# Kernel optimization log

Hardware: AMD Instinct MI355X
Metric: run time of the kernel (lower is better)

The kernel has to match this reference:

```python
import jax, jax.numpy as jnp
import numpy as np

B, T, IN = 32, 64, 90
U, SEG = 4, 16          # conductor steps, decoder steps per segment (T = U*SEG)
H1, HC, HD, Z = 2048, 1024, 1024, 512


def _lstm_layer(x, wih, whh, bih, bhh, h0=None, c0=None, reverse=False):
    """PyTorch-convention LSTM layer. x: [B,T,D]. Returns (ys [B,T,H], final h [B,H])."""
    b = x.shape[0]
    H = whh.shape[1]
    # precompute input projection for all timesteps: [T,B,4H]
    xp = jnp.swapaxes(jnp.einsum('btd,gd->btg', x, wih) + bih, 0, 1)
    if h0 is None:
        h0 = jnp.zeros((b, H), x.dtype)
        c0 = h0
    def step(carry, xt):
        h, c = carry
        g = xt + h @ whh.T + bhh
        i, f, gg, o = jnp.split(g, 4, axis=-1)  # torch gate order i,f,g,o
        c = jax.nn.sigmoid(f) * c + jax.nn.sigmoid(i) * jnp.tanh(gg)
        h = jax.nn.sigmoid(o) * jnp.tanh(c)
        return (h, c), h
    (h, c), ys = jax.lax.scan(step, (h0, c0), xp, reverse=reverse)
    return jnp.swapaxes(ys, 0, 1), h


def _cell(xin, h, c, wih, whh, bih, bhh):
    g = xin @ wih.T + bih + h @ whh.T + bhh
    i, f, gg, o = jnp.split(g, 4, axis=-1)
    c = jax.nn.sigmoid(f) * c + jax.nn.sigmoid(i) * jnp.tanh(gg)
    h = jax.nn.sigmoid(o) * jnp.tanh(c)
    return h, c


def setup_inputs() -> dict:
    key = jax.random.key(0)
    ks = iter(jax.random.split(key, 64))
    def p(*shape):
        return jax.random.normal(next(ks), shape, dtype=jnp.float32) * 0.02
    inp = {}
    inp['x'] = jax.random.normal(next(ks), (B, T, IN), dtype=jnp.float32)
    inp['eps'] = jax.random.normal(next(ks), (B, Z), dtype=jnp.float32)
    # encoder bi-LSTM: 2 layers x 2 directions
    for name, d in [('e0f', IN), ('e0b', IN), ('e1f', 2 * H1), ('e1b', 2 * H1)]:
        inp[name + '_wih'] = p(4 * H1, d)
        inp[name + '_whh'] = p(4 * H1, H1)
        inp[name + '_bih'] = p(4 * H1)
        inp[name + '_bhh'] = p(4 * H1)
    inp['wm'] = p(Z, 2 * H1); inp['bm'] = p(Z)
    inp['ws'] = p(Z, 2 * H1); inp['bs'] = p(Z)
    inp['w2'] = p(4 * HC, Z); inp['b2'] = p(4 * HC)
    # conductor LSTM: 2 layers, input size 1
    for name, d in [('c0', 1), ('c1', HC)]:
        inp[name + '_wih'] = p(4 * HC, d)
        inp[name + '_whh'] = p(4 * HC, HC)
        inp[name + '_bih'] = p(4 * HC)
        inp[name + '_bhh'] = p(4 * HC)
    inp['w3'] = p(4 * HD, HC); inp['b3'] = p(4 * HD)
    # two decoder LSTMCells
    for name, d in [('d1', HC + IN), ('d2', HD)]:
        inp[name + '_wih'] = p(4 * HD, d)
        inp[name + '_whh'] = p(4 * HD, HD)
        inp[name + '_bih'] = p(4 * HD)
        inp[name + '_bhh'] = p(4 * HD)
    inp['w4'] = p(IN, HD); inp['b4'] = p(IN)
    return inp


def reference(x, eps,
              e0f_wih, e0f_whh, e0f_bih, e0f_bhh,
              e0b_wih, e0b_whh, e0b_bih, e0b_bhh,
              e1f_wih, e1f_whh, e1f_bih, e1f_bhh,
              e1b_wih, e1b_whh, e1b_bih, e1b_bhh,
              wm, bm, ws, bs, w2, b2,
              c0_wih, c0_whh, c0_bih, c0_bhh,
              c1_wih, c1_whh, c1_bih, c1_bhh,
              w3, b3,
              d1_wih, d1_whh, d1_bih, d1_bhh,
              d2_wih, d2_whh, d2_bih, d2_bhh,
              w4, b4):
    b = x.shape[0]
    # ----- encode: 2-layer bidirectional LSTM, take layer-1 fwd/bwd final h -----
    y0f, _ = _lstm_layer(x, e0f_wih, e0f_whh, e0f_bih, e0f_bhh)
    y0b, _ = _lstm_layer(x, e0b_wih, e0b_whh, e0b_bih, e0b_bhh, reverse=True)
    y0 = jnp.concatenate([y0f, y0b], axis=2)  # [B,T,2*H1]
    _, hf = _lstm_layer(y0, e1f_wih, e1f_whh, e1f_bih, e1f_bhh)
    _, hb = _lstm_layer(y0, e1b_wih, e1b_whh, e1b_bih, e1b_bhh, reverse=True)
    ht = jnp.concatenate([hf, hb], axis=1)  # [B,4096]
    z_mean = ht @ wm.T + bm
    z_std = jnp.log1p(jnp.exp(ht @ ws.T + bs))  # softplus as in source
    z = z_mean + eps * z_std
    # ----- conductor -----
    t = jnp.tanh(z @ w2.T + b2)
    h1, h2, c1, c2 = jnp.split(t, 4, axis=1)  # source order: h1,h2,c1,c2
    zin = jnp.zeros((b, U, 1), x.dtype)
    yc0, _ = _lstm_layer(zin, c0_wih, c0_whh, c0_bih, c0_bhh, h1, c1)
    emb, _ = _lstm_layer(yc0, c1_wih, c1_whh, c1_bih, c1_bhh, h2, c2)  # [B,U,HC]
    def segment(prev, e):
        s = jnp.tanh(e @ w3.T + b3)
        sh1, sh2, sc1, sc2 = jnp.split(s, 4, axis=1)
        def step(carry, _):
            dh1, dc1, dh2, dc2, p = carry
            inp = jnp.concatenate([e, p], axis=1)
            dh1, dc1 = _cell(inp, dh1, dc1, d1_wih, d1_whh, d1_bih, d1_bhh)
            dh2, dc2 = _cell(dh1, dh2, dc2, d2_wih, d2_whh, d2_bih, d2_bhh)
            p = dh2 @ w4.T + b4
            return (dh1, dc1, dh2, dc2, p), p
        carry, outs = jax.lax.scan(step, (sh1, sc1, sh2, sc2, prev), None, length=SEG)
        return carry[4], outs  # outs: [SEG,B,IN]
    prev0 = jnp.zeros((b, IN), x.dtype)
    _, outs = jax.lax.scan(segment, prev0, jnp.swapaxes(emb, 0, 1))  # [U,SEG,B,IN]
    out = jnp.transpose(outs.reshape(U * SEG, b, IN), (1, 0, 2))  # [B,T,IN]
    out = jax.nn.softmax(out, axis=2)
    return out, z_mean, z_std
```

## Files before the change

kernel.cpp:

```cpp
#include <hip/hip_runtime.h>
#include <hip/hip_cooperative_groups.h>
#include <math.h>

#define BB 32
#define TT 64
#define INPW 90
#define NU 4
#define NH1 2048
#define NHC 1024
#define NHD 1024
#define NZ 512
#define BSTRIDE 12800

typedef unsigned short u16;
typedef __attribute__((ext_vector_type(8))) short short8;
typedef __attribute__((ext_vector_type(4))) float f32x4;
typedef __attribute__((ext_vector_type(4))) unsigned uv4;
typedef __attribute__((ext_vector_type(2))) unsigned uv2;

__device__ __forceinline__ float sigf(float v) { return 1.0f / (1.0f + __expf(-v)); }

__device__ __forceinline__ u16 f2bf(float f) {
  unsigned u = __float_as_uint(f);
  unsigned r = (u + 0x7FFFu + ((u >> 16) & 1u)) >> 16;
  return (u16)r;
}
__device__ __forceinline__ float bf2f(u16 b) { return __uint_as_float(((unsigned)b) << 16); }

__device__ __forceinline__ void cstore16(u16* p, uv4 v) {
  asm volatile("global_store_dwordx4 %0, %1, off sc0 sc1" :: "v"(p), "v"(v) : "memory");
}
__device__ __forceinline__ void cstore8(u16* p, uv2 v) {
  asm volatile("global_store_dwordx2 %0, %1, off sc0 sc1" :: "v"(p), "v"(v) : "memory");
}
__device__ __forceinline__ void cstore4(unsigned* p, unsigned v) {
  asm volatile("global_store_dword %0, %1, off sc0 sc1" :: "v"(p), "v"(v) : "memory");
}
__device__ __forceinline__ unsigned fload(const unsigned* p) {
  unsigned r;
  asm volatile("global_load_dword %0, %1, off sc0 sc1\n\ts_waitcnt vmcnt(0)"
               : "=v"(r) : "v"(p) : "memory");
  return r;
}
__device__ __forceinline__ void gbar(unsigned* base) {
  asm volatile("s_waitcnt vmcnt(0)" ::: "memory");
  __syncthreads();
  if (threadIdx.x == 0) {
    unsigned old = atomicAdd(&base[(blockIdx.x & 15) * 512], 1u);
    if (old == 15u) {
      unsigned m = atomicAdd(&base[16 * 512], 1u);
      if (m == 15u) {
#pragma unroll
        for (int k = 0; k < 8; ++k) cstore4(&base[(17 + k) * 512], 1u);
        asm volatile("s_waitcnt vmcnt(0)" ::: "memory");
      }
    }
    while (!fload(&base[(17 + (blockIdx.x & 7)) * 512])) __builtin_amdgcn_s_sleep(2);
  }
  __syncthreads();
}

__device__ __forceinline__ void gload16(const u16* g, u16* l) {
  __builtin_amdgcn_global_load_lds(
      (const __attribute__((address_space(1))) unsigned*)g,
      (__attribute__((address_space(3))) unsigned*)l, 16, 0, 0);
}

__global__ void cvt_flat(const float* __restrict__ s, u16* __restrict__ d, long n) {
  long i = ((long)blockIdx.x * 256 + threadIdx.x) * 4;
  if (i >= n) return;
  float4 v = *(const float4*)&s[i];
  d[i] = f2bf(v.x); d[i + 1] = f2bf(v.y); d[i + 2] = f2bf(v.z); d[i + 3] = f2bf(v.w);
}

__global__ void cvt_pad(const float* __restrict__ s, int sld, int cols,
                        u16* __restrict__ d, int dld, int rows) {
  int c = blockIdx.x * blockDim.x + threadIdx.x;
  int r = blockIdx.y;
  if (c >= dld) return;
  d[(long)r * dld + c] = (c < cols) ? f2bf(s[(long)r * sld + c]) : (u16)0;
}

__global__ void cvt_permrow(const float* __restrict__ s, int sld, int cols,
                            u16* __restrict__ d, int dld, int H) {
  int c = blockIdx.x * blockDim.x + threadIdx.x;
  int r = blockIdx.y;
  if (c >= dld) return;
  long sr = (long)(r & 3) * H + (r >> 2);
  d[(long)r * dld + c] = (c < cols) ? f2bf(s[sr * sld + c]) : (u16)0;
}

__global__ void bias_perm(const float* __restrict__ s, float* __restrict__ d, int H) {
  int n = blockIdx.x * 256 + threadIdx.x;
  if (n >= 4 * H) return;
  d[n] = s[(long)(n & 3) * H + (n >> 2)];
}

__global__ void xcvt(const float* __restrict__ x, u16* __restrict__ xb) {
  int r = blockIdx.x, c = threadIdx.x;
  int b = r & 31, t = r >> 5;
  float v = (c < INPW) ? x[((long)b * TT + t) * INPW + c] : 0.0f;
  xb[(long)r * 128 + c] = f2bf(v);
}

__global__ void w4t_k(const float* __restrict__ w4, u16* __restrict__ w4tb) {
  int k = blockIdx.x, n = threadIdx.x;
  w4tb[(long)k * 128 + n] = (n < INPW) ? f2bf(w4[(long)n * NHD + k]) : (u16)0;
}

__global__ void bfuse_k(const float* __restrict__ d1_wih, const float* __restrict__ b4,
                        float* __restrict__ bfuse) {
  int r = blockIdx.x * 256 + threadIdx.x;
  if (r >= 4096) return;
  float s = 0.0f;
  for (int n = 0; n < INPW; ++n) s += d1_wih[(long)r * 1114 + 1024 + n] * b4[n];
  bfuse[r] = s;
}

__global__ __launch_bounds__(256) void gemm_bf(
    const u16* __restrict__ A, int lda, const u16* __restrict__ Bw, int ldb,
    const float* __restrict__ bias, u16* __restrict__ C, int ldc, int K, int mode,
    int nbm, int nbn) {
  __shared__ u16 Asm[2][128 * 64];
  __shared__ u16 Bsm[2][128 * 64];
  const int tid = threadIdx.x;
  const int w = tid >> 6, l = tid & 63, q = (tid >> 4) & 3, ln = tid & 15;
  const int wm = w & 1, wn = w >> 1;
  int fid = blockIdx.x;
  int sidx = fid >> 3, xcd = fid & 7;
  int bm, bn;
  if ((nbm & 7) == 0) { bn = sidx % nbn; bm = xcd * (nbm >> 3) + sidx / nbn; }
  else if ((nbn & 7) == 0) { bm = sidx % nbm; bn = xcd * (nbn >> 3) + sidx / nbm; }
  else { bm = fid % nbm; bn = fid / nbm; }
  const long am0 = (long)bm * 128;
  const long bn0 = (long)bn * 128;
  const u16* Ap0 = A + am0 * lda;
  const u16* Bp0 = Bw + bn0 * ldb;
  f32x4 acc[4][4] = {};

  auto stage = [&](int b, int k0) {
#pragma unroll
    for (int i = 0; i < 4; ++i) {
      int row = (w * 4 + i) * 8 + (l >> 3);
      int col = (((l & 7) ^ (row & 7)) << 3) + k0;
      gload16(Ap0 + (long)row * lda + col, &Asm[b][(w * 4 + i) * 512]);
      gload16(Bp0 + (long)row * ldb + col, &Bsm[b][(w * 4 + i) * 512]);
    }
  };

  const int kt = K >> 6;
  stage(0, 0);
  asm volatile("s_waitcnt vmcnt(0)" ::: "memory");
  __syncthreads();
  int buf = 0;
  for (int t = 0; t < kt; ++t) {
    if (t + 1 < kt) stage(buf ^ 1, (t + 1) << 6);
#pragma unroll
    for (int kh = 0; kh < 2; ++kh) {
      short8 af[4], bg[4];
#pragma unroll
      for (int tt2 = 0; tt2 < 4; ++tt2) {
        int arr = wm * 64 + tt2 * 16 + ln;
        af[tt2] = *(short8*)&Asm[buf][arr * 64 + (((q + 4 * kh) ^ (arr & 7)) << 3)];
        int brr = wn * 64 + tt2 * 16 + ln;
        bg[tt2] = *(short8*)&Bsm[buf][brr * 64 + (((q + 4 * kh) ^ (brr & 7)) << 3)];
      }
#pragma unroll
      for (int mt = 0; mt < 4; ++mt)
#pragma unroll
        for (int nt = 0; nt < 4; ++nt)
          acc[mt][nt] = __builtin_amdgcn_mfma_f32_16x16x32_bf16(af[mt], bg[nt], acc[mt][nt], 0, 0, 0);
    }
    asm volatile("s_waitcnt vmcnt(0)" ::: "memory");
    __syncthreads();
    buf ^= 1;
  }
#pragma unroll
  for (int nt = 0; nt < 4; ++nt) {
    long n = bn0 + wn * 64 + nt * 16 + ln;
    float bv = bias ? bias[n] : 0.0f;
#pragma unroll
    for (int mt = 0; mt < 4; ++mt) {
#pragma unroll
      for (int r = 0; r < 4; ++r) {
        long m = am0 + wm * 64 + mt * 16 + (q << 2) + r;
        long dst;
        if (mode == 0) {
          dst = m * ldc + n;
        } else if (mode == 1) {
          dst = (((m >> 5) * 256 + (n >> 5)) * 32 + (m & 31)) * 32 + (n & 31);
        } else {
          dst = ((n >> 4) * 128 + m) * 16 + (n & 15);
        }
        C[dst] = f2bf(acc[mt][nt][r] + bv);
      }
    }
  }
}

__global__ __launch_bounds__(256) void gemm128(
    const float* __restrict__ A, int lda, const float* __restrict__ W, int ldw,
    const float* __restrict__ bias, float* __restrict__ C, int ldc,
    int M, int K, int act, u16* __restrict__ Cb) {
  __shared__ float As[16][132];
  __shared__ float Bs[16][132];
  const int tid = threadIdx.x;
  const int bm = blockIdx.x, bn = blockIdx.y;
  const int tm = tid & 15, tn = tid >> 4;
  float acc[8][8] = {};
  for (int k0 = 0; k0 < K; k0 += 16) {
#pragma unroll
    for (int it = 0; it < 2; ++it) {
      int e = it * 256 + tid;
      int r = e >> 2, c4 = (e & 3) * 4;
      int m = bm * 128 + r;
      float4 v = make_float4(0.f, 0.f, 0.f, 0.f);
      if (m < M) v = *(const float4*)&A[(long)m * lda + k0 + c4];
      As[c4 + 0][r] = v.x; As[c4 + 1][r] = v.y; As[c4 + 2][r] = v.z; As[c4 + 3][r] = v.w;
      int n = bn * 128 + r;
      float4 w = *(const float4*)&W[(long)n * ldw + k0 + c4];
      Bs[c4 + 0][r] = w.x; Bs[c4 + 1][r] = w.y; Bs[c4 + 2][r] = w.z; Bs[c4 + 3][r] = w.w;
    }
    __syncthreads();
#pragma unroll
    for (int kk = 0; kk < 16; ++kk) {
      float4 a0 = *(const float4*)&As[kk][tm * 8];
      float4 a1 = *(const float4*)&As[kk][tm * 8 + 4];
      float4 b0 = *(const float4*)&Bs[kk][tn * 8];
      float4 b1 = *(const float4*)&Bs[kk][tn * 8 + 4];
      float av[8] = {a0.x, a0.y, a0.z, a0.w, a1.x, a1.y, a1.z, a1.w};
      float bv[8] = {b0.x, b0.y, b0.z, b0.w, b1.x, b1.y, b1.z, b1.w};
#pragma unroll
      for (int i = 0; i < 8; ++i)
#pragma unroll
        for (int j = 0; j < 8; ++j)
          acc[i][j] += av[i] * bv[j];
    }
    __syncthreads();
  }
#pragma unroll
  for (int i = 0; i < 8; ++i) {
    int m = bm * 128 + tm * 8 + i;
    if (m >= M) continue;
#pragma unroll
    for (int j = 0; j < 8; ++j) {
      int n = bn * 128 + tn * 8 + j;
      float v = acc[i][j] + bias[n];
      if (act == 1) v = tanhf(v);
      else if (act == 2) v = log1pf(__expf(v));
      C[(long)m * ldc + n] = v;
      if (Cb) Cb[(long)m * ldc + n] = f2bf(v);
    }
  }
}

__global__ __launch_bounds__(256) void latgemm(
    const float* __restrict__ A, const float* __restrict__ W,
    const float* __restrict__ bias, float* __restrict__ C, int act) {
  __shared__ float red[16][16][32];
  const int tid = threadIdx.x;
  const int c = tid & 15, ksl = tid >> 4;
  const int n = blockIdx.x * 16 + c;
  const float* wp = W + (long)n * 4096 + ksl * 256;
  const float* ap = A + ksl * 256;
  float acc[32];
#pragma unroll
  for (int r = 0; r < 32; ++r) acc[r] = 0.f;
  for (int k = 0; k < 256; k += 4) {
    float4 wv = *(const float4*)(wp + k);
#pragma unroll
    for (int r = 0; r < 32; ++r) {
      float4 hv = *(const float4*)(ap + (long)r * 4096 + k);
      acc[r] += hv.x * wv.x + hv.y * wv.y + hv.z * wv.z + hv.w * wv.w;
    }
  }
#pragma unroll
  for (int r = 0; r < 32; ++r) red[ksl][c][r] = acc[r];
  __syncthreads();
  for (int o = tid; o < 512; o += 256) {
    int cc = o >> 5, r = o & 31;
    float s = 0.f;
#pragma unroll
    for (int p = 0; p < 16; ++p) s += red[p][cc][r];
    s += bias[blockIdx.x * 16 + cc];
    if (act == 2) s = log1pf(__expf(s));
    C[(long)r * 512 + blockIdx.x * 16 + cc] = s;
  }
}

__global__ void zcalc_kernel(const float* __restrict__ zm, const float* __restrict__ zs,
                             const float* __restrict__ eps, float* __restrict__ z) {
  int e = blockIdx.x * 256 + threadIdx.x;
  if (e < BB * NZ) z[e] = zm[e] + eps[e] * zs[e];
}

__global__ void softmax_kernel(float* __restrict__ out) {
  long row = blockIdx.x;
  float* p = out + row * INPW;
  int lane = threadIdx.x;
  float v0 = (lane < INPW) ? p[lane] : -1e30f;
  float v1 = (lane + 64 < INPW) ? p[lane + 64] : -1e30f;
  float m = fmaxf(v0, v1);
#pragma unroll
  for (int off = 32; off > 0; off >>= 1) m = fmaxf(m, __shfl_xor(m, off));
  float e0 = (lane < INPW) ? __expf(v0 - m) : 0.0f;
  float e1 = (lane + 64 < INPW) ? __expf(v1 - m) : 0.0f;
  float sum = e0 + e1;
#pragma unroll
  for (int off = 32; off > 0; off >>= 1) sum += __shfl_xor(sum, off);
  float inv = 1.0f / sum;
  if (lane < INPW) p[lane] = e0 * inv;
  if (lane + 64 < INPW) p[lane + 64] = e1 * inv;
}

struct EncArgs {
  const u16* whh[2];
  const u16* xp[2];
  const float* bhh[2];
  u16* y0b;
  u16* h1a[2];
  float* htb;
  unsigned* bar;
  int layer;
};

__global__ __launch_bounds__(512) void enc_coop(EncArgs A) {
  __shared__ u16 Wl[2 * 64 * 64 * 8];
  __shared__ __align__(16) float red[4 * 64 * 4];
  __shared__ __align__(16) u16 hstage[32][8];
  const int tid = threadIdx.x;
  const int w = tid >> 6, l = tid & 63;
  const int rt = w & 1, bh = (w >> 1) & 1, kh = w >> 2;
  const int kg = l >> 4, b0 = l & 15;
  const int j0 = blockIdx.x * 8;
  const int jout = j0 + rt * 4 + kg;
  const int batch = bh * 16 + b0;
  float* redp = &red[((bh * 2 + rt) * 64 + l) * 4];

  for (int dir = 0; dir < 2; ++dir) {
    __syncthreads();
    {
      const u16* W = A.whh[dir];
      for (int e = tid; e < 8192; e += 512) {
        int ert = e >> 12, es = (e >> 6) & 63, el = e & 63;
        int etr = el & 15;
        long gr = (long)(etr & 3) * 2048 + j0 + ert * 4 + (etr >> 2);
        *(uint4*)&Wl[((ert * 64 + es) * 64 + el) * 8] =
            *(const uint4*)&W[gr * 2048 + (el >> 4) * 8 + (long)es * 32];
      }
    }
    __syncthreads();
    const float* bhh = A.bhh[dir];
    const u16* xp = A.xp[dir];
    const float bi0 = bhh[jout], bi1 = bhh[2048 + jout],
                bi2 = bhh[4096 + jout], bi3 = bhh[6144 + jout];
    float creg = 0.f;
    ushort4 xv4 = make_ushort4(0, 0, 0, 0);
    if (kh == 0) {
      int tt0 = dir ? 63 : 0;
      xv4 = *(const ushort4*)(xp + ((((long)tt0 * 256 + blockIdx.x) * 32 + batch) * 32)
                              + (rt * 4 + kg) * 4);
    }
    for (int s = 0; s < 64; ++s) {
      if (s) gbar(A.bar + (long)(dir * 63 + (s - 1)) * BSTRIDE);
      const int tt = dir ? 63 - s : s;
      f32x4 acc = {0.f, 0.f, 0.f, 0.f};
      if (s) {
        const u16* hb; long hld;
        if (A.layer == 0) {
          int tp = dir ? tt + 1 : tt - 1;
          hb = A.y0b + (long)tp * 32 * 4096 + dir * 2048;
          hld = 4096;
        } else {
          hb = A.h1a[dir] + (long)(s - 1) * 32 * 2048;
          hld = 2048;
        }
        const u16* xv = hb + (long)batch * hld + kg * 8;
        for (int ks = kh * 32; ks < kh * 32 + 32; ks += 8) {
          uint4 bv[8]; short8 av[8];
#pragma unroll
          for (int uu = 0; uu < 8; ++uu)
            bv[uu] = *(const uint4*)(xv + (long)(ks + uu) * 32);
#pragma unroll
          for (int uu = 0; uu < 8; ++uu)
            av[uu] = *(const short8*)&Wl[((rt * 64 + ks + uu) * 64 + l) * 8];
#pragma unroll
          for (int uu = 0; uu < 8; ++uu)
            acc = __builtin_amdgcn_mfma_f32_16x16x32_bf16(av[uu], *(short8*)&bv[uu], acc, 0, 0, 0);
        }
      }
      if (kh) *(f32x4*)redp = acc;
      __syncthreads();
      if (kh == 0) {
        f32x4 o = *(f32x4*)redp;
        float g0 = acc[0] + o[0] + bi0 + bf2f(xv4.x);
        float g1 = acc[1] + o[1] + bi1 + bf2f(xv4.y);
        float g2 = acc[2] + o[2] + bi2 + bf2f(xv4.z);
        float g3 = acc[3] + o[3] + bi3 + bf2f(xv4.w);
        float iv = sigf(g0), fv = sigf(g1), gv = tanhf(g2), ov = sigf(g3);
        float c = fv * creg + iv * gv;
        creg = c;
        float h = ov * tanhf(c);
        hstage[batch][rt * 4 + kg] = f2bf(h);
        if (A.layer == 1 && s == 63) A.htb[batch * 4096 + dir * 2048 + jout] = h;
      }
      __syncthreads();
      if (tid < 32) {
        uv4 v = *(const uv4*)&hstage[tid][0];
        u16* dst;
        if (A.layer == 0) dst = &A.y0b[((long)tt * 32 + tid) * 4096 + dir * 2048 + j0];
        else dst = &A.h1a[dir][((long)s * 32 + tid) * 2048 + j0];
        cstore16(dst, v);
      }
      if (kh == 0 && s < 63) {
        int ttn = dir ? 62 - s : s + 1;
        xv4 = *(const ushort4*)(xp + ((((long)ttn * 256 + blockIdx.x) * 32 + batch) * 32)
                                + (rt * 4 + kg) * 4);
      }
    }
  }
}

__device__ __forceinline__ void stage_w1024(u16* Wl, int m, const u16* W, int j0, int tid) {
  for (int e = tid; e < 2048; e += 512) {
    int kh = e >> 10, s = (e >> 6) & 15, el = e & 63;
    int tr = el & 15;
    long gr = (long)(tr & 3) * 1024 + j0 + (tr >> 2);
    *(uint4*)&Wl[(((m * 2 + kh) * 16 + s) * 64 + el) * 8] =
        *(const uint4*)&W[gr * 1024 + kh * 512 + (el >> 4) * 8 + s * 32];
  }
}

__device__ __forceinline__ void cell1024_lds(
    const u16* Wl, int m0, int m1,
    int j0, int tid, float* red, u16* hstage,
    const u16* X0, long x0ld,
    const u16* X1, long x1ld,
    float xg0, float xg1, float xg2, float xg3,
    float b0, float b1, float b2, float b3,
    float co, float* crp,
    u16* hout, long hld, float* houtf, long hfld) {
  const int w = tid >> 6, l = tid & 63;
  const int bh = w & 1, kh = w >> 1;
  const int kg = l >> 4;
  const int koff = kh * 256 + kg * 8;
  const int batch = bh * 16 + (l & 15);
  const int sbase = (kh >> 1) * 16 + (kh & 1) * 8;
  const int jout = j0 + kg;
  f32x4 acc = {0.f, 0.f, 0.f, 0.f};
  if (X0) {
    const u16* xpt = X0 + (long)batch * x0ld + koff;
    const int sb = m0 * 32 + sbase;
    uint4 bv[8]; short8 av[8];
#pragma unroll
    for (int uu = 0; uu < 8; ++uu) bv[uu] = *(const uint4*)(xpt + (long)uu * 32);
#pragma unroll
    for (int uu = 0; uu < 8; ++uu) av[uu] = *(const short8*)&Wl[((sb + uu) * 64 + l) * 8];
#pragma unroll
    for (int uu = 0; uu < 8; ++uu)
      acc = __builtin_amdgcn_mfma_f32_16x16x32_bf16(av[uu], *(short8*)&bv[uu], acc, 0, 0, 0);
  }
  if (X1) {
    const u16* xpt = X1 + (long)batch * x1ld + koff;
    const int sb = m1 * 32 + sbase;
    uint4 bv[8]; short8 av[8];
#pragma unroll
    for (int uu = 0; uu < 8; ++uu) bv[uu] = *(const uint4*)(xpt + (long)uu * 32);
#pragma unroll
    for (int uu = 0; uu < 8; ++uu) av[uu] = *(const short8*)&Wl[((sb + uu) * 64 + l) * 8];
#pragma unroll
    for (int uu = 0; uu < 8; ++uu)
      acc = __builtin_amdgcn_mfma_f32_16x16x32_bf16(av[uu], *(short8*)&bv[uu], acc, 0, 0, 0);
  }
  if (kh) *(f32x4*)&red[((kh - 1) * 2 + bh) * 256 + l * 4] = acc;
  __syncthreads();
  if (kh == 0) {
#pragma unroll
    for (int p = 0; p < 3; ++p) {
      f32x4 o = *(f32x4*)&red[(p * 2 + bh) * 256 + l * 4];
      acc[0] += o[0]; acc[1] += o[1]; acc[2] += o[2]; acc[3] += o[3];
    }
    float g0 = acc[0] + b0 + xg0;
    float g1 = acc[1] + b1 + xg1;
    float g2 = acc[2] + b2 + xg2;
    float g3 = acc[3] + b3 + xg3;
    float iv = sigf(g0), fv = sigf(g1), gv = tanhf(g2), ov = sigf(g3);
    float c = fv * co + iv * gv;
    *crp = c;
    float h = ov * tanhf(c);
    hstage[batch * 4 + kg] = f2bf(h);
    if (houtf) houtf[(long)batch * hfld + jout] = h;
  }
  __syncthreads();
  if (tid < 32) {
    uv2 v = *(const uv2*)&hstage[tid * 4];
    cstore8(&hout[(long)tid * hld + j0], v);
  }
}

struct CondArgs {
  const u16 *c0h, *c1w, *c1h, *tvecb;
  const float* tvec;
  u16 *yc0b, *embb;
  float* embf;
  const float *b0i, *b0h, *b1i, *b1h;
  unsigned* bar;
};
__global__ __launch_bounds__(512) void cond_coop(CondArgs A) {
  __shared__ u16 Wl[3 * 32 * 512];
  __shared__ __align__(16) float red[6 * 256];
  __shared__ __align__(16) u16 hstage[128];
  const int j0 = blockIdx.x * 4;
  const int tid = threadIdx.x;
  const int w = tid >> 6, l = tid & 63;
  const int bh = w & 1;
  const int jout = j0 + (l >> 4);
  const int batch = bh * 16 + (l & 15);
  stage_w1024(Wl, 0, A.c0h, j0, tid);
  stage_w1024(Wl, 1, A.c1w, j0, tid);
  stage_w1024(Wl, 2, A.c1h, j0, tid);
  const float cb00 = A.b0i[jout] + A.b0h[jout];
  const float cb01 = A.b0i[1024 + jout] + A.b0h[1024 + jout];
  const float cb02 = A.b0i[2048 + jout] + A.b0h[2048 + jout];
  const float cb03 = A.b0i[3072 + jout] + A.b0h[3072 + jout];
  const float cb10 = A.b1i[jout] + A.b1h[jout];
  const float cb11 = A.b1i[1024 + jout] + A.b1h[1024 + jout];
  const float cb12 = A.b1i[2048 + jout] + A.b1h[2048 + jout];
  const float cb13 = A.b1i[3072 + jout] + A.b1h[3072 + jout];
  const float c0init = A.tvec[2048 + (long)batch * 4096 + jout];
  const float c1init = A.tvec[3072 + (long)batch * 4096 + jout];
  __syncthreads();
  float cr0 = c0init, cr1 = c1init;
  int bi = 0;
  for (int u = 0; u < NU; ++u) {
    cell1024_lds(Wl, 0, -1, j0, tid, red, hstage,
                 u ? A.yc0b + (long)(u - 1) * 32 * 1024 : A.tvecb, u ? 1024 : 4096,
                 nullptr, 0,
                 0.f, 0.f, 0.f, 0.f,
                 cb00, cb01, cb02, cb03,
                 cr0, &cr0,
                 A.yc0b + (long)u * 32 * 1024, 1024, nullptr, 0);
    gbar(A.bar + (long)(bi++) * BSTRIDE);
    cell1024_lds(Wl, 1, 2, j0, tid, red, hstage,
                 A.yc0b + (long)u * 32 * 1024, 1024,
                 u ? A.embb + (long)(u - 1) * 32 * 1024 : A.tvecb + 1024, u ? 1024 : 4096,
                 0.f, 0.f, 0.f, 0.f,
                 cb10, cb11, cb12, cb13,
                 cr1, &cr1,
                 A.embb + (long)u * 32 * 1024, 1024, A.embf + (long)u * 32 * 1024, 1024);
    if (u < NU - 1) gbar(A.bar + (long)(bi++) * BSTRIDE);
  }
}

struct DecArgs {
  const u16 *d1h, *wfuse, *d2w, *d2h, *xeb, *sallb;
  const float* sall;
  u16 *dh1all, *dh2all;
  const float *bfuse, *b1h, *b2i, *b2h;
  unsigned* bar;
};
__global__ __launch_bounds__(512) void dec_coop(DecArgs A) {
  __shared__ u16 Wl[4 * 32 * 512];
  __shared__ __align__(16) float red[6 * 256];
  __shared__ __align__(16) u16 hstage[128];
  const int j0 = blockIdx.x * 4;
  const int tid = threadIdx.x;
  const int w = tid >> 6, l = tid & 63;
  const int bh = w & 1;
  const int kg = l >> 4;
  const int jout = j0 + kg;
  const int batch = bh * 16 + (l & 15);
  stage_w1024(Wl, 0, A.d1h, j0, tid);
  stage_w1024(Wl, 1, A.wfuse, j0, tid);
  stage_w1024(Wl, 2, A.d2w, j0, tid);
  stage_w1024(Wl, 3, A.d2h, j0, tid);
  const float b1z0 = A.b1h[jout], b1z1 = A.b1h[1024 + jout],
              b1z2 = A.b1h[2048 + jout], b1z3 = A.b1h[3072 + jout];
  const float b1n0 = b1z0 + A.bfuse[jout], b1n1 = b1z1 + A.bfuse[1024 + jout],
              b1n2 = b1z2 + A.bfuse[2048 + jout], b1n3 = b1z3 + A.bfuse[3072 + jout];
  const float b20 = A.b2i[jout] + A.b2h[jout];
  const float b21 = A.b2i[1024 + jout] + A.b2h[1024 + jout];
  const float b22 = A.b2i[2048 + jout] + A.b2h[2048 + jout];
  const float b23 = A.b2i[3072 + jout] + A.b2h[3072 + jout];
  const u16* xqb = A.xeb + (long)blockIdx.x * 128 * 16;
  ushort4 xq4 = *(const ushort4*)(xqb + (long)batch * 16 + kg * 4);
  float con1 = A.sall[(long)batch * 4096 + 2048 + jout];
  float con2 = A.sall[(long)batch * 4096 + 3072 + jout];
  __syncthreads();
  float cr1 = 0.f, cr2 = 0.f;
  int bi = 0;
  for (int t = 0; t < TT; ++t) {
    const int u = t >> 4, sg = t & 15;
    if (sg == 0) { cr1 = con1; cr2 = con2; }
    cell1024_lds(Wl, 0, 1, j0, tid, red, hstage,
                 sg ? A.dh1all + (long)(t - 1) * 32 * 1024 : A.sallb + (long)u * 32 * 4096,
                 sg ? 1024 : 4096,
                 t ? A.dh2all + (long)(t - 1) * 32 * 1024 : nullptr, 1024,
                 bf2f(xq4.x), bf2f(xq4.y), bf2f(xq4.z), bf2f(xq4.w),
                 t ? b1n0 : b1z0, t ? b1n1 : b1z1, t ? b1n2 : b1z2, t ? b1n3 : b1z3,
                 cr1, &cr1,
                 A.dh1all + (long)t * 32 * 1024, 1024, nullptr, 0);
    gbar(A.bar + (long)(bi++) * BSTRIDE);
    cell1024_lds(Wl, 2, 3, j0, tid, red, hstage,
                 A.dh1all + (long)t * 32 * 1024, 1024,
                 sg ? A.dh2all + (long)(t - 1) * 32 * 1024 : A.sallb + (long)u * 32 * 4096 + 1024,
                 sg ? 1024 : 4096,
                 0.f, 0.f, 0.f, 0.f,
                 b20, b21, b22, b23,
                 cr2, &cr2,
                 A.dh2all + (long)t * 32 * 1024, 1024, nullptr, 0);
    if (sg == 15 && u < 3) {
      xq4 = *(const ushort4*)(xqb + (long)(u + 1) * 32 * 16 + (long)batch * 16 + kg * 4);
      con1 = A.sall[(long)(u + 1) * 32 * 4096 + (long)batch * 4096 + 2048 + jout];
      con2 = A.sall[(long)(u + 1) * 32 * 4096 + (long)batch * 4096 + 3072 + jout];
    }
    if (t < TT - 1) gbar(A.bar + (long)(bi++) * BSTRIDE);
  }
}

__global__ __launch_bounds__(256) void proj_all(const u16* __restrict__ dh2all,
                                                const u16* __restrict__ w4b,
                                                const float* __restrict__ b4,
                                                float* __restrict__ out) {
  __shared__ u16 hs[8 * 1024];
  const int r0 = blockIdx.x * 8;
  for (int e = threadIdx.x; e < 1024; e += 256)
    ((uint4*)hs)[e] = ((const uint4*)(dh2all + (long)r0 * 1024))[e];
  __syncthreads();
  for (int o = threadIdx.x; o < 8 * INPW; o += 256) {
    int rr = o / INPW, n = o % INPW;
    const u16* wr = w4b + (long)n * 1024;
    const u16* hr = hs + rr * 1024;
    float s = 0.0f;
    for (int k = 0; k < 1024; ++k) s += bf2f(hr[k]) * bf2f(wr[k]);
    int row = r0 + rr;
    int tt = row >> 5, b = row & 31;
    out[((long)b * TT + tt) * INPW + n] = s + b4[n];
  }
}

extern "C" void kernel_launch(void* const* d_in, const int* in_sizes, int n_in,
                              void* d_out, int out_size, void* d_ws, size_t ws_size,
                              hipStream_t stream) {
  (void)in_sizes; (void)n_in; (void)out_size;
  const float* x        = (const float*)d_in[0];
  const float* eps      = (const float*)d_in[1];
  const float* e0f_wih  = (const float*)d_in[2];
  const float* e0f_whh  = (const float*)d_in[3];
  const float* e0f_bih  = (const float*)d_in[4];
  const float* e0f_bhh  = (const float*)d_in[5];
  const float* e0b_wih  = (const float*)d_in[6];
  const float* e0b_whh  = (const float*)d_in[7];
  const float* e0b_bih  = (const float*)d_in[8];
  const float* e0b_bhh  = (const float*)d_in[9];
  const float* e1f_wih  = (const float*)d_in[10];
  const float* e1f_whh  = (const float*)d_in[11];
  const float* e1f_bih  = (const float*)d_in[12];
  const float* e1f_bhh  = (const float*)d_in[13];
  const float* e1b_wih  = (const float*)d_in[14];
  const float* e1b_whh  = (const float*)d_in[15];
  const float* e1b_bih  = (const float*)d_in[16];
  const float* e1b_bhh  = (const float*)d_in[17];
  const float* wm  = (const float*)d_in[18];
  const float* bm  = (const float*)d_in[19];
  const float* wsw = (const float*)d_in[20];
  const float* bsv = (const float*)d_in[21];
  const float* w2  = (const float*)d_in[22];
  const float* b2  = (const float*)d_in[23];
  const float* c0_whh = (const float*)d_in[25];
  const float* c0_bih = (const float*)d_in[26];
  const float* c0_bhh = (const float*)d_in[27];
  const float* c1_wih = (const float*)d_in[28];
  const float* c1_whh = (const float*)d_in[29];
  const float* c1_bih = (const float*)d_in[30];
  const float* c1_bhh = (const float*)d_in[31];
  const float* w3 = (const float*)d_in[32];
  const float* b3 = (const float*)d_in[33];
  const float* d1_wih = (const float*)d_in[34];
  const float* d1_whh = (const float*)d_in[35];
  const float* d1_bih = (const float*)d_in[36];
  const float* d1_bhh = (const float*)d_in[37];
  const float* d2_wih = (const float*)d_in[38];
  const float* d2_whh = (const float*)d_in[39];
  const float* d2_bih = (const float*)d_in[40];
  const float* d2_bhh = (const float*)d_in[41];
  const float* w4 = (const float*)d_in[42];
  const float* b4 = (const float*)d_in[43];

  float* out = (float*)d_out;
  float* zm_out = out + (size_t)BB * TT * INPW;
  float* zs_out = zm_out + BB * NZ;

  char* wbase = (char*)d_ws;
  size_t cur = 0;
  auto AL = [&](size_t bytes) -> void* {
    void* p = wbase + cur;
    cur = (cur + bytes + 255) & ~(size_t)255;
    return p;
  };
  u16* xb    = (u16*)AL(2048L * 128 * 2);
  u16* e0wf  = (u16*)AL(8192L * 128 * 2);
  u16* e0wb  = (u16*)AL(8192L * 128 * 2);
  u16* e0hf  = (u16*)AL(8192L * 2048 * 2);
  u16* e0hb  = (u16*)AL(8192L * 2048 * 2);
  u16* e1wf  = (u16*)AL(8192L * 4096 * 2);
  u16* e1wb  = (u16*)AL(8192L * 4096 * 2);
  u16* e1hf  = (u16*)AL(8192L * 2048 * 2);
  u16* e1hb  = (u16*)AL(8192L * 2048 * 2);
  u16* c0h   = (u16*)AL(4096L * 1024 * 2);
  u16* c1w   = (u16*)AL(4096L * 1024 * 2);
  u16* c1h   = (u16*)AL(4096L * 1024 * 2);
  u16* d1we  = (u16*)AL(4096L * 1024 * 2);
  u16* d1wp  = (u16*)AL(4096L * 128 * 2);
  u16* d1h   = (u16*)AL(4096L * 1024 * 2);
  u16* d2w   = (u16*)AL(4096L * 1024 * 2);
  u16* d2h   = (u16*)AL(4096L * 1024 * 2);
  u16* w4b   = (u16*)AL(90L * 1024 * 2);
  u16* w4tb  = (u16*)AL(1024L * 128 * 2);
  u16* wfuse = (u16*)AL(4096L * 1024 * 2);
  float* bfuse = (float*)AL(4096L * 4);
  float* pb_e0f = (float*)AL(8192L * 4);
  float* pb_e0b = (float*)AL(8192L * 4);
  float* pb_e1f = (float*)AL(8192L * 4);
  float* pb_e1b = (float*)AL(8192L * 4);
  float* pb_d1  = (float*)AL(4096L * 4);
  u16* xp0f  = (u16*)AL(2048L * 8192 * 2);
  u16* xp0b  = (u16*)AL(2048L * 8192 * 2);
  u16* y0b   = (u16*)AL(2048L * 4096 * 2);
  u16* xp1f  = (u16*)AL(2048L * 8192 * 2);
  u16* xp1b  = (u16*)AL(2048L * 8192 * 2);
  u16* h1af  = (u16*)AL(64L * 32 * 2048 * 2);
  u16* h1ab  = (u16*)AL(64L * 32 * 2048 * 2);
  u16* tvecb = (u16*)AL(32L * 4096 * 2);
  u16* yc0b  = (u16*)AL(4L * 32 * 1024 * 2);
  u16* embb  = (u16*)AL(4L * 32 * 1024 * 2);
  u16* sallb = (u16*)AL(128L * 4096 * 2);
  u16* xeb   = (u16*)AL(128L * 4096 * 2);
  u16* dh1all= (u16*)AL(64L * 32 * 1024 * 2);
  u16* dh2all= (u16*)AL(64L * 32 * 1024 * 2);
  float* htb  = (float*)AL(32L * 4096 * 4);
  float* zbuf = (float*)AL(32L * 512 * 4);
  float* tvec = (float*)AL(32L * 4096 * 4);
  float* embf = (float*)AL(128L * 1024 * 4);
  float* sall = (float*)AL(128L * 4096 * 4);
  unsigned* barp = (unsigned*)AL(400L * BSTRIDE * 4);
  if (cur > ws_size) return;

  unsigned* bar_enc0 = barp;
  unsigned* bar_enc1 = barp + 128L * BSTRIDE;
  unsigned* bar_cond = barp + 256L * BSTRIDE;
  unsigned* bar_dec  = barp + 264L * BSTRIDE;

  auto cf = [&](const float* s, u16* d, long n) {
    cvt_flat<<<dim3((unsigned)((n / 4 + 255) / 256)), 256, 0, stream>>>(s, d, n);
  };
  cf(e0f_whh, e0hf, 8192L * 2048);
  cf(e0b_whh, e0hb, 8192L * 2048);
  cf(e1f_whh, e1hf, 8192L * 2048);
  cf(e1b_whh, e1hb, 8192L * 2048);
  cf(c0_whh, c0h, 4096L * 1024);
  cf(c1_wih, c1w, 4096L * 1024);
  cf(c1_whh, c1h, 4096L * 1024);
  cf(d1_whh, d1h, 4096L * 1024);
  cf(d2_wih, d2w, 4096L * 1024);
  cf(d2_whh, d2h, 4096L * 1024);
  cf(w4, w4b, 90L * 1024);
  cvt_permrow<<<dim3(1, 8192), 128, 0, stream>>>(e0f_wih, 90, 90, e0wf, 128, 2048);
  cvt_permrow<<<dim3(1, 8192), 128, 0, stream>>>(e0b_wih, 90, 90, e0wb, 128, 2048);
  cvt_permrow<<<dim3(16, 8192), 256, 0, stream>>>(e1f_wih, 4096, 4096, e1wf, 4096, 2048);
  cvt_permrow<<<dim3(16, 8192), 256, 0, stream>>>(e1b_wih, 4096, 4096, e1wb, 4096, 2048);
  cvt_permrow<<<dim3(4, 4096), 256, 0, stream>>>(d1_wih, 1114, 1024, d1we, 1024, 1024);
  bias_perm<<<dim3(32), 256, 0, stream>>>(e0f_bih, pb_e0f, 2048);
  bias_perm<<<dim3(32), 256, 0, stream>>>(e0b_bih, pb_e0b, 2048);
  bias_perm<<<dim3(32), 256, 0, stream>>>(e1f_bih, pb_e1f, 2048);
  bias_perm<<<dim3(32), 256, 0, stream>>>(e1b_bih, pb_e1b, 2048);
  bias_perm<<<dim3(16), 256, 0, stream>>>(d1_bih, pb_d1, 1024);
  cvt_pad<<<dim3(1, 4096), 128, 0, stream>>>(d1_wih + 1024, 1114, 90, d1wp, 128, 4096);
  xcvt<<<dim3(2048), 128, 0, stream>>>(x, xb);
  w4t_k<<<dim3(1024), 128, 0, stream>>>(w4, w4tb);
  bfuse_k<<<dim3(16), 256, 0, stream>>>(d1_wih, b4, bfuse);
  hipMemsetAsync(barp, 0, 400L * BSTRIDE * 4, stream);

  gemm_bf<<<dim3(256), 256, 0, stream>>>(d1wp, 128, w4tb, 128, nullptr, wfuse, 1024, 128, 0, 32, 8);
  gemm_bf<<<dim3(1024), 256, 0, stream>>>(xb, 128, e0wf, 128, pb_e0f, xp0f, 8192, 128, 1, 16, 64);
  gemm_bf<<<dim3(1024), 256, 0, stream>>>(xb, 128, e0wb, 128, pb_e0b, xp0b, 8192, 128, 1, 16, 64);

  {
    EncArgs ea{};
    ea.whh[0] = e0hf; ea.whh[1] = e0hb;
    ea.xp[0] = xp0f; ea.xp[1] = xp0b;
    ea.bhh[0] = e0f_bhh; ea.bhh[1] = e0b_bhh;
    ea.y0b = y0b; ea.h1a[0] = h1af; ea.h1a[1] = h1ab; ea.htb = htb;
    ea.bar = bar_enc0; ea.layer = 0;
    void* args[] = {&ea};
    (void)hipLaunchCooperativeKernel((void*)enc_coop, dim3(256), dim3(512), args, 0, stream);
  }

  gemm_bf<<<dim3(1024), 256, 0, stream>>>(y0b, 4096, e1wf, 4096, pb_e1f, xp1f, 8192, 4096, 1, 16, 64);
  gemm_bf<<<dim3(1024), 256, 0, stream>>>(y0b, 4096, e1wb, 4096, pb_e1b, xp1b, 8192, 4096, 1, 16, 64);

  {
    EncArgs ea{};
    ea.whh[0] = e1hf; ea.whh[1] = e1hb;
    ea.xp[0] = xp1f; ea.xp[1] = xp1b;
    ea.bhh[0] = e1f_bhh; ea.bhh[1] = e1b_bhh;
    ea.y0b = y0b; ea.h1a[0] = h1af; ea.h1a[1] = h1ab; ea.htb = htb;
    ea.bar = bar_enc1; ea.layer = 1;
    void* args[] = {&ea};
    (void)hipLaunchCooperativeKernel((void*)enc_coop, dim3(256), dim3(512), args, 0, stream);
  }

  latgemm<<<dim3(32), 256, 0, stream>>>(htb, wm, bm, zm_out, 0);
  latgemm<<<dim3(32), 256, 0, stream>>>(htb, wsw, bsv, zs_out, 2);
  zcalc_kernel<<<dim3(64), 256, 0, stream>>>(zm_out, zs_out, eps, zbuf);
  gemm128<<<dim3(1, 32), 256, 0, stream>>>(zbuf, 512, w2, 512, b2, tvec, 4096, 32, 512, 1, tvecb);

  {
    CondArgs ca{};
    ca.c0h = c0h; ca.c1w = c1w; ca.c1h = c1h;
    ca.tvecb = tvecb; ca.tvec = tvec;
    ca.yc0b = yc0b; ca.embb = embb; ca.embf = embf;
    ca.b0i = c0_bih; ca.b0h = c0_bhh; ca.b1i = c1_bih; ca.b1h = c1_bhh;
    ca.bar = bar_cond;
    void* args[] = {&ca};
    (void)hipLaunchCooperativeKernel((void*)cond_coop, dim3(256), dim3(512), args, 0, stream);
  }

  gemm128<<<dim3(1, 32), 256, 0, stream>>>(embf, 1024, w3, 1024, b3, sall, 4096, 128, 1024, 1, sallb);
  gemm_bf<<<dim3(32), 256, 0, stream>>>(embb, 1024, d1we, 1024, pb_d1, xeb, 4096, 1024, 2, 1, 32);

  {
    DecArgs da{};
    da.d1h = d1h; da.wfuse = wfuse; da.d2w = d2w; da.d2h = d2h;
    da.xeb = xeb; da.sallb = sallb; da.sall = sall;
    da.dh1all = dh1all; da.dh2all = dh2all;
    da.bfuse = bfuse; da.b1h = d1_bhh; da.b2i = d2_bih; da.b2h = d2_bhh;
    da.bar = bar_dec;
    void* args[] = {&da};
    (void)hipLaunchCooperativeKernel((void*)dec_coop, dim3(256), dim3(512), args, 0, stream);
  }

  proj_all<<<dim3(256), 256, 0, stream>>>(dh2all, w4b, b4, out);
  softmax_kernel<<<dim3(BB * TT), 64, 0, stream>>>(out);
}
```

Before: 4.900 ms.

## Replace LDS h staging with wave shuffles and batch conversion launches

The recurrent cells no longer stage each new hidden state in shared memory followed by a block barrier. Instead, lanes gather bf16 h values with wave shuffles, and 16 lanes per wave write 8-byte coherent stores directly, which removes one __syncthreads per cell step on the latency-bound recurrent path. Separately, eleven weight conversion launches are merged into one grid-stride kernel and five bias-permutation launches into one, to reduce launch overhead. The encoder now issues more, smaller stores (dwordx2 instead of dwordx4).

```diff
diff --git a/kernel.cpp b/kernel.cpp
--- a/kernel.cpp
+++ b/kernel.cpp
@@ -27,9 +27,6 @@
 }
 __device__ __forceinline__ float bf2f(u16 b) { return __uint_as_float(((unsigned)b) << 16); }
 
-__device__ __forceinline__ void cstore16(u16* p, uv4 v) {
-  asm volatile("global_store_dwordx4 %0, %1, off sc0 sc1" :: "v"(p), "v"(v) : "memory");
-}
 __device__ __forceinline__ void cstore8(u16* p, uv2 v) {
   asm volatile("global_store_dwordx2 %0, %1, off sc0 sc1" :: "v"(p), "v"(v) : "memory");
 }
@@ -66,11 +63,25 @@
       (__attribute__((address_space(3))) unsigned*)l, 16, 0, 0);
 }
 
-__global__ void cvt_flat(const float* __restrict__ s, u16* __restrict__ d, long n) {
-  long i = ((long)blockIdx.x * 256 + threadIdx.x) * 4;
-  if (i >= n) return;
-  float4 v = *(const float4*)&s[i];
-  d[i] = f2bf(v.x); d[i + 1] = f2bf(v.y); d[i + 2] = f2bf(v.z); d[i + 3] = f2bf(v.w);
+struct CvtJobs { const float* s[12]; u16* d[12]; long n[12]; int cnt; };
+__global__ void cvt_multi(CvtJobs J) {
+  long stride = (long)gridDim.x * 256 * 4;
+  for (int j = 0; j < J.cnt; ++j) {
+    const float* s = J.s[j]; u16* d = J.d[j]; long n = J.n[j];
+    for (long i = ((long)blockIdx.x * 256 + threadIdx.x) * 4; i < n; i += stride) {
+      float4 v = *(const float4*)&s[i];
+      d[i] = f2bf(v.x); d[i + 1] = f2bf(v.y); d[i + 2] = f2bf(v.z); d[i + 3] = f2bf(v.w);
+    }
+  }
+}
+
+struct BPJobs { const float* s[5]; float* d[5]; int H[5]; int cnt; };
+__global__ void bias_perm5(BPJobs J) {
+  for (int j = 0; j < J.cnt; ++j) {
+    int tot = 4 * J.H[j];
+    for (int n = blockIdx.x * 256 + threadIdx.x; n < tot; n += gridDim.x * 256)
+      J.d[j][n] = J.s[j][(long)(n & 3) * J.H[j] + (n >> 2)];
+  }
 }
 
 __global__ void cvt_pad(const float* __restrict__ s, int sld, int cols,
@@ -88,12 +99,6 @@
   if (c >= dld) return;
   long sr = (long)(r & 3) * H + (r >> 2);
   d[(long)r * dld + c] = (c < cols) ? f2bf(s[sr * sld + c]) : (u16)0;
-}
-
-__global__ void bias_perm(const float* __restrict__ s, float* __restrict__ d, int H) {
-  int n = blockIdx.x * 256 + threadIdx.x;
-  if (n >= 4 * H) return;
-  d[n] = s[(long)(n & 3) * H + (n >> 2)];
 }
 
 __global__ void xcvt(const float* __restrict__ x, u16* __restrict__ xb) {
@@ -327,7 +332,6 @@
 __global__ __launch_bounds__(512) void enc_coop(EncArgs A) {
   __shared__ u16 Wl[2 * 64 * 64 * 8];
   __shared__ __align__(16) float red[4 * 64 * 4];
-  __shared__ __align__(16) u16 hstage[32][8];
   const int tid = threadIdx.x;
   const int w = tid >> 6, l = tid & 63;
   const int rt = w & 1, bh = (w >> 1) & 1, kh = w >> 2;
@@ -401,21 +405,27 @@
         float c = fv * creg + iv * gv;
         creg = c;
         float h = ov * tanhf(c);
-        hstage[batch][rt * 4 + kg] = f2bf(h);
         if (A.layer == 1 && s == 63) A.htb[batch * 4096 + dir * 2048 + jout] = h;
-      }
-      __syncthreads();
-      if (tid < 32) {
-        uv4 v = *(const uv4*)&hstage[tid][0];
-        u16* dst;
-        if (A.layer == 0) dst = &A.y0b[((long)tt * 32 + tid) * 4096 + dir * 2048 + j0];
-        else dst = &A.h1a[dir][((long)s * 32 + tid) * 2048 + j0];
-        cstore16(dst, v);
-      }
-      if (kh == 0 && s < 63) {
-        int ttn = dir ? 62 - s : s + 1;
-        xv4 = *(const ushort4*)(xp + ((((long)ttn * 256 + blockIdx.x) * 32 + batch) * 32)
-                                + (rt * 4 + kg) * 4);
+        unsigned hbits = f2bf(h);
+        unsigned p0 = __shfl((int)hbits, (l & 15));
+        unsigned p1 = __shfl((int)hbits, (l & 15) + 16);
+        unsigned p2 = __shfl((int)hbits, (l & 15) + 32);
+        unsigned p3 = __shfl((int)hbits, (l & 15) + 48);
+        if (l < 16) {
+          int b2 = bh * 16 + l;
+          uv2 v;
+          v.x = (p0 & 0xffffu) | (p1 << 16);
+          v.y = (p2 & 0xffffu) | (p3 << 16);
+          u16* dst;
+          if (A.layer == 0) dst = &A.y0b[((long)tt * 32 + b2) * 4096 + dir * 2048 + j0 + rt * 4];
+          else dst = &A.h1a[dir][((long)s * 32 + b2) * 2048 + j0 + rt * 4];
+          cstore8(dst, v);
+        }
+        if (s < 63) {
+          int ttn = dir ? 62 - s : s + 1;
+          xv4 = *(const ushort4*)(xp + ((((long)ttn * 256 + blockIdx.x) * 32 + batch) * 32)
+                                  + (rt * 4 + kg) * 4);
+        }
       }
     }
   }
@@ -433,7 +443,7 @@
 
 __device__ __forceinline__ void cell1024_lds(
     const u16* Wl, int m0, int m1,
-    int j0, int tid, float* red, u16* hstage,
+    int j0, int tid, float* red,
     const u16* X0, long x0ld,
     const u16* X1, long x1ld,
     float xg0, float xg1, float xg2, float xg3,
@@ -488,13 +498,19 @@
     float c = fv * co + iv * gv;
     *crp = c;
     float h = ov * tanhf(c);
-    hstage[batch * 4 + kg] = f2bf(h);
     if (houtf) houtf[(long)batch * hfld + jout] = h;
-  }
-  __syncthreads();
-  if (tid < 32) {
-    uv2 v = *(const uv2*)&hstage[tid * 4];
-    cstore8(&hout[(long)tid * hld + j0], v);
+    unsigned hbits = f2bf(h);
+    unsigned p0 = __shfl((int)hbits, (l & 15));
+    unsigned p1 = __shfl((int)hbits, (l & 15) + 16);
+    unsigned p2 = __shfl((int)hbits, (l & 15) + 32);
+    unsigned p3 = __shfl((int)hbits, (l & 15) + 48);
+    if (l < 16) {
+      int b2 = bh * 16 + l;
+      uv2 v;
+      v.x = (p0 & 0xffffu) | (p1 << 16);
+      v.y = (p2 & 0xffffu) | (p3 << 16);
+      cstore8(&hout[(long)b2 * hld + j0], v);
+    }
   }
 }
 
@@ -509,7 +525,6 @@
 __global__ __launch_bounds__(512) void cond_coop(CondArgs A) {
   __shared__ u16 Wl[3 * 32 * 512];
   __shared__ __align__(16) float red[6 * 256];
-  __shared__ __align__(16) u16 hstage[128];
   const int j0 = blockIdx.x * 4;
   const int tid = threadIdx.x;
   const int w = tid >> 6, l = tid & 63;
@@ -533,7 +548,7 @@
   float cr0 = c0init, cr1 = c1init;
   int bi = 0;
   for (int u = 0; u < NU; ++u) {
-    cell1024_lds(Wl, 0, -1, j0, tid, red, hstage,
+    cell1024_lds(Wl, 0, -1, j0, tid, red,
                  u ? A.yc0b + (long)(u - 1) * 32 * 1024 : A.tvecb, u ? 1024 : 4096,
                  nullptr, 0,
                  0.f, 0.f, 0.f, 0.f,
@@ -541,7 +556,7 @@
                  cr0, &cr0,
                  A.yc0b + (long)u * 32 * 1024, 1024, nullptr, 0);
     gbar(A.bar + (long)(bi++) * BSTRIDE);
-    cell1024_lds(Wl, 1, 2, j0, tid, red, hstage,
+    cell1024_lds(Wl, 1, 2, j0, tid, red,
                  A.yc0b + (long)u * 32 * 1024, 1024,
                  u ? A.embb + (long)(u - 1) * 32 * 1024 : A.tvecb + 1024, u ? 1024 : 4096,
                  0.f, 0.f, 0.f, 0.f,
@@ -562,7 +577,6 @@
 __global__ __launch_bounds__(512) void dec_coop(DecArgs A) {
   __shared__ u16 Wl[4 * 32 * 512];
   __shared__ __align__(16) float red[6 * 256];
-  __shared__ __align__(16) u16 hstage[128];
   const int j0 = blockIdx.x * 4;
   const int tid = threadIdx.x;
   const int w = tid >> 6, l = tid & 63;
@@ -592,7 +606,7 @@
   for (int t = 0; t < TT; ++t) {
     const int u = t >> 4, sg = t & 15;
     if (sg == 0) { cr1 = con1; cr2 = con2; }
-    cell1024_lds(Wl, 0, 1, j0, tid, red, hstage,
+    cell1024_lds(Wl, 0, 1, j0, tid, red,
                  sg ? A.dh1all + (long)(t - 1) * 32 * 1024 : A.sallb + (long)u * 32 * 4096,
                  sg ? 1024 : 4096,
                  t ? A.dh2all + (long)(t - 1) * 32 * 1024 : nullptr, 1024,
@@ -601,7 +615,7 @@
                  cr1, &cr1,
                  A.dh1all + (long)t * 32 * 1024, 1024, nullptr, 0);
     gbar(A.bar + (long)(bi++) * BSTRIDE);
-    cell1024_lds(Wl, 2, 3, j0, tid, red, hstage,
+    cell1024_lds(Wl, 2, 3, j0, tid, red,
                  A.dh1all + (long)t * 32 * 1024, 1024,
                  sg ? A.dh2all + (long)(t - 1) * 32 * 1024 : A.sallb + (long)u * 32 * 4096 + 1024,
                  sg ? 1024 : 4096,
@@ -751,30 +765,39 @@
   unsigned* bar_cond = barp + 256L * BSTRIDE;
   unsigned* bar_dec  = barp + 264L * BSTRIDE;
 
-  auto cf = [&](const float* s, u16* d, long n) {
-    cvt_flat<<<dim3((unsigned)((n / 4 + 255) / 256)), 256, 0, stream>>>(s, d, n);
-  };
-  cf(e0f_whh, e0hf, 8192L * 2048);
-  cf(e0b_whh, e0hb, 8192L * 2048);
-  cf(e1f_whh, e1hf, 8192L * 2048);
-  cf(e1b_whh, e1hb, 8192L * 2048);
-  cf(c0_whh, c0h, 4096L * 1024);
-  cf(c1_wih, c1w, 4096L * 1024);
-  cf(c1_whh, c1h, 4096L * 1024);
-  cf(d1_whh, d1h, 4096L * 1024);
-  cf(d2_wih, d2w, 4096L * 1024);
-  cf(d2_whh, d2h, 4096L * 1024);
-  cf(w4, w4b, 90L * 1024);
+  {
+    CvtJobs J{};
+    int c = 0;
+    auto add = [&](const float* s, u16* d, long n) { J.s[c] = s; J.d[c] = d; J.n[c] = n; ++c; };
+    add(e0f_whh, e0hf, 8192L * 2048);
+    add(e0b_whh, e0hb, 8192L * 2048);
+    add(e1f_whh, e1hf, 8192L * 2048);
+    add(e1b_whh, e1hb, 8192L * 2048);
+    add(c0_whh, c0h, 4096L * 1024);
+    add(c1_wih, c1w, 4096L * 1024);
+    add(c1_whh, c1h, 4096L * 1024);
+    add(d1_whh, d1h, 4096L * 1024);
+    add(d2_wih, d2w, 4096L * 1024);
+    add(d2_whh, d2h, 4096L * 1024);
+    add(w4, w4b, 90L * 1024);
+    J.cnt = c;
+    cvt_multi<<<dim3(2048), 256, 0, stream>>>(J);
+  }
   cvt_permrow<<<dim3(1, 8192), 128, 0, stream>>>(e0f_wih, 90, 90, e0wf, 128, 2048);
   cvt_permrow<<<dim3(1, 8192), 128, 0, stream>>>(e0b_wih, 90, 90, e0wb, 128, 2048);
   cvt_permrow<<<dim3(16, 8192), 256, 0, stream>>>(e1f_wih, 4096, 4096, e1wf, 4096, 2048);
   cvt_permrow<<<dim3(16, 8192), 256, 0, stream>>>(e1b_wih, 4096, 4096, e1wb, 4096, 2048);
   cvt_permrow<<<dim3(4, 4096), 256, 0, stream>>>(d1_wih, 1114, 1024, d1we, 1024, 1024);
-  bias_perm<<<dim3(32), 256, 0, stream>>>(e0f_bih, pb_e0f, 2048);
-  bias_perm<<<dim3(32), 256, 0, stream>>>(e0b_bih, pb_e0b, 2048);
-  bias_perm<<<dim3(32), 256, 0, stream>>>(e1f_bih, pb_e1f, 2048);
-  bias_perm<<<dim3(32), 256, 0, stream>>>(e1b_bih, pb_e1b, 2048);
-  bias_perm<<<dim3(16), 256, 0, stream>>>(d1_bih, pb_d1, 1024);
+  {
+    BPJobs J{};
+    J.s[0] = e0f_bih; J.d[0] = pb_e0f; J.H[0] = 2048;
+    J.s[1] = e0b_bih; J.d[1] = pb_e0b; J.H[1] = 2048;
+    J.s[2] = e1f_bih; J.d[2] = pb_e1f; J.H[2] = 2048;
+    J.s[3] = e1b_bih; J.d[3] = pb_e1b; J.H[3] = 2048;
+    J.s[4] = d1_bih;  J.d[4] = pb_d1;  J.H[4] = 1024;
+    J.cnt = 5;
+    bias_perm5<<<dim3(32), 256, 0, stream>>>(J);
+  }
   cvt_pad<<<dim3(1, 4096), 128, 0, stream>>>(d1_wih + 1024, 1114, 90, d1wp, 128, 4096);
   xcvt<<<dim3(2048), 128, 0, stream>>>(x, xb);
   w4t_k<<<dim3(1024), 128, 0, stream>>>(w4, w4tb);
```

Result: no change. 4.916 ms (+0.3%).
